# Kernel optimization log

Measured on AMD Instinct MI355X. Metric: run time of the kernel, lower is better.

The kernel has to match this reference:

```python
import jax, jax.numpy as jnp
import numpy as np

N_NODES = 100000

def _gcn_norm(edge_index, num_nodes):
    # PyG GCNConv: add self-loops, symmetric normalization deg^-1/2 A_hat deg^-1/2
    loop = jnp.arange(num_nodes, dtype=edge_index.dtype)
    src = jnp.concatenate([edge_index[0], loop])  # [E+N]
    dst = jnp.concatenate([edge_index[1], loop])  # [E+N]
    deg = jax.ops.segment_sum(jnp.ones(dst.shape[0], jnp.float32), dst, num_segments=num_nodes)
    dis = jnp.where(deg > 0, jax.lax.rsqrt(deg), 0.0)
    norm = dis[src] * dis[dst]  # [E+N]
    return src, dst, norm

def _gcn_layer(x, W, b, src, dst, norm, num_nodes):
    xw = x @ W                                   # [N, H] dense GEMM first (out_dim <= in_dim)
    msg = xw[src] * norm[:, None]                # gather + scale per edge
    out = jax.ops.segment_sum(msg, dst, num_segments=num_nodes)  # scatter-add
    return out + b

def setup_inputs() -> dict:
    key = jax.random.key(0)
    ks = jax.random.split(key, 6)
    E = 1600000
    return {
        "x": jax.random.normal(ks[0], (N_NODES, 512), jnp.float32),
        "edge_index": jax.random.randint(ks[1], (2, E), 0, N_NODES, dtype=jnp.int64),
        "W1": jax.random.normal(ks[2], (512, 256), jnp.float32) * 0.04,
        "b1": jnp.zeros((256,), jnp.float32),
        "W2": jax.random.normal(ks[3], (256, 256), jnp.float32) * 0.06,
        "b2": jnp.zeros((256,), jnp.float32),
        "fc_w": jax.random.normal(ks[4], (256, 128), jnp.float32) * 0.06,
        "fc_b": jnp.zeros((128,), jnp.float32),
    }

def reference(x, edge_index, W1, b1, W2, b2, fc_w, fc_b):
    src, dst, norm = _gcn_norm(edge_index, N_NODES)
    h = jax.nn.relu(_gcn_layer(x, W1, b1, src, dst, norm, N_NODES))
    h = jax.nn.relu(_gcn_layer(h, W2, b2, src, dst, norm, N_NODES))
    return h @ fc_w + fc_b
```

## Files before the change

kernel.cpp:

```cpp
#include <hip/hip_runtime.h>


#define N_NODES 100000
constexpr int D_IN  = 512;
constexpr int D_H   = 256;
constexpr int D_OUT = 128;

typedef _Float16 f16x8 __attribute__((ext_vector_type(8)));
typedef _Float16 f16x4 __attribute__((ext_vector_type(4)));
typedef float f32x4 __attribute__((ext_vector_type(4)));


__global__ __launch_bounds__(256) void deg_count_k(const int* __restrict__ dst,
                                                   int* __restrict__ deg, int E) {
  int i = blockIdx.x * 256 + threadIdx.x;
  if (i < E) atomicAdd(&deg[dst[i]], 1);
}

__global__ __launch_bounds__(256) void dis_k(const int* __restrict__ deg,
                                             float* __restrict__ dis, int n) {
  int i = blockIdx.x * 256 + threadIdx.x;
  if (i < n) dis[i] = rsqrtf((float)deg[i] + 1.0f);
}

__global__ __launch_bounds__(256) void scan1_k(const int* __restrict__ deg,
                                               int* __restrict__ off,
                                               int* __restrict__ bsum, int n) {
  __shared__ int ts[256];
  const int tid = threadIdx.x;
  const int base = blockIdx.x * 1024 + tid * 4;
  int v[4];
#pragma unroll
  for (int t = 0; t < 4; ++t) v[t] = (base + t < n) ? deg[base + t] : 0;
  const int tot = v[0] + v[1] + v[2] + v[3];
  ts[tid] = tot;
  __syncthreads();
  for (int o = 1; o < 256; o <<= 1) {
    int t = (tid >= o) ? ts[tid - o] : 0;
    __syncthreads();
    ts[tid] += t;
    __syncthreads();
  }
  int run = ts[tid] - tot;
#pragma unroll
  for (int t = 0; t < 4; ++t) {
    if (base + t < n) off[base + t] = run;
    run += v[t];
  }
  if (tid == 255) bsum[blockIdx.x] = ts[255];
}

__global__ __launch_bounds__(128) void scan2_k(int* __restrict__ bsum, int nb) {
  __shared__ int ts[128];
  const int tid = threadIdx.x;
  const int v = (tid < nb) ? bsum[tid] : 0;
  ts[tid] = v;
  __syncthreads();
  for (int o = 1; o < 128; o <<= 1) {
    int t = (tid >= o) ? ts[tid - o] : 0;
    __syncthreads();
    ts[tid] += t;
    __syncthreads();
  }
  if (tid < nb) bsum[tid] = ts[tid] - v;
}

__global__ __launch_bounds__(256) void scan3_k(int* __restrict__ off,
                                               const int* __restrict__ bsum,
                                               int n, int E) {
  int i = blockIdx.x * 256 + threadIdx.x;
  if (i < n) off[i] += bsum[i >> 10];
  if (i == 0) off[n] = E;
}

__global__ __launch_bounds__(256) void fill_k(const int* __restrict__ src,
                                              const int* __restrict__ dst,
                                              const int* __restrict__ off,
                                              int* __restrict__ cursor,
                                              int* __restrict__ ssorted, int E) {
  int e = blockIdx.x * 256 + threadIdx.x;
  if (e < E) {
    int d = dst[e];
    int p = off[d] + atomicAdd(&cursor[d], 1);
    ssorted[p] = src[e];
  }
}

__global__ __launch_bounds__(256) void wtrans_k(const float* __restrict__ W,
                                                _Float16* __restrict__ T,
                                                int K, int logN) {
  int i = blockIdx.x * 256 + threadIdx.x;
  if (i >= (K << logN)) return;
  int k = i >> logN, n = i & ((1 << logN) - 1);
  T[(size_t)n * K + k] = (_Float16)W[i];
}

template<int BN, bool CONVERT_A, bool OUT_Y>
__global__ __launch_bounds__(512, 4) void gemm_pipe_k(
    const float* __restrict__ Af32,
    const _Float16* __restrict__ A16,
    const _Float16* __restrict__ Bt,
    const float* __restrict__ bias,
    const float* __restrict__ dis,
    float* __restrict__ C,
    _Float16* __restrict__ Y,
    int M, int K) {
  constexpr int BM = 128, BK = 32;
  constexpr int FN = BN / 64;
  constexpr int NB = BN / 128;
  constexpr int EPAD = 4;

  __shared__ __align__(16) _Float16 smem[2 * (BM + BN) * BK];
  _Float16* As = smem;
  _Float16* Bs = smem + 2 * BM * BK;
  float* epi = (float*)smem;

  const int tid  = threadIdx.x;
  const int wid  = tid >> 6, lane = tid & 63;
  const int wm   = wid >> 2, wn = wid & 3;
  const int l15  = lane & 15, l16 = lane >> 4;
  const int row0 = blockIdx.y * BM;

  f32x4 acc[4][FN];
#pragma unroll
  for (int i = 0; i < 4; ++i)
#pragma unroll
    for (int j = 0; j < FN; ++j) acc[i][j] = (f32x4){0.f, 0.f, 0.f, 0.f};

  const int arow = tid >> 2;
  const int ak8  = (tid & 3) << 3;
  float4 areg0, areg1;
  f16x8  a16reg;
  f16x8  breg[NB];

  const int nsteps = K >> 5;

  auto stage_load = [&](int kt) {
    const int gr = row0 + arow;
    if constexpr (CONVERT_A) {
      if (gr < M) {
        const float* ap = Af32 + (size_t)gr * K + kt + ak8;
        areg0 = *(const float4*)ap;
        areg1 = *(const float4*)(ap + 4);
      } else {
        areg0 = make_float4(0.f, 0.f, 0.f, 0.f);
        areg1 = make_float4(0.f, 0.f, 0.f, 0.f);
      }
    } else {
      if (gr < M) a16reg = *(const f16x8*)(A16 + (size_t)gr * K + kt + ak8);
      else        a16reg = (f16x8){0, 0, 0, 0, 0, 0, 0, 0};
    }
#pragma unroll
    for (int it = 0; it < NB; ++it) {
      int idx = tid + it * 512;
      int n = idx >> 2, k8 = (idx & 3) << 3;
      breg[it] = *(const f16x8*)(Bt + (size_t)n * K + kt + k8);
    }
  };

  auto stage_write = [&](int buf) {
    _Float16* as = As + buf * (BM * BK);
    _Float16* bs = Bs + buf * (BN * BK);
    if constexpr (CONVERT_A) {
      f16x8 v;
      v[0] = (_Float16)areg0.x; v[1] = (_Float16)areg0.y;
      v[2] = (_Float16)areg0.z; v[3] = (_Float16)areg0.w;
      v[4] = (_Float16)areg1.x; v[5] = (_Float16)areg1.y;
      v[6] = (_Float16)areg1.z; v[7] = (_Float16)areg1.w;
      *(f16x8*)&as[arow * BK + ak8] = v;
    } else {
      *(f16x8*)&as[arow * BK + ak8] = a16reg;
    }
#pragma unroll
    for (int it = 0; it < NB; ++it) {
      int idx = tid + it * 512;
      int n = idx >> 2, k8 = (idx & 3) << 3;
      *(f16x8*)&bs[n * BK + k8] = breg[it];
    }
  };

  stage_load(0);
  stage_write(0);
  if (nsteps > 1) stage_load(BK);
  __syncthreads();

  for (int t = 0; t < nsteps; ++t) {
    const int buf = t & 1;
    const _Float16* as = As + buf * (BM * BK);
    const _Float16* bs = Bs + buf * (BN * BK);

    f16x8 a[4], b[FN];
#pragma unroll
    for (int i = 0; i < 4; ++i)
      a[i] = *(const f16x8*)&as[(wm * 64 + i * 16 + l15) * BK + l16 * 8];
#pragma unroll
    for (int j = 0; j < FN; ++j)
      b[j] = *(const f16x8*)&bs[(wn * (FN * 16) + j * 16 + l15) * BK + l16 * 8];

#pragma unroll
    for (int i = 0; i < 4; ++i)
#pragma unroll
      for (int j = 0; j < FN; ++j)
        acc[i][j] = __builtin_amdgcn_mfma_f32_16x16x32_f16(a[i], b[j], acc[i][j], 0, 0, 0);

    if (t + 1 < nsteps) {
      stage_write(buf ^ 1);
      if (t + 2 < nsteps) stage_load((t + 2) << 5);
    }
    __syncthreads();
  }

  constexpr int ESTR = BN + EPAD;
  constexpr int CPT  = BN / 16;
#pragma unroll
  for (int c = 0; c < 4; ++c) {
    if (wm == (c >> 1)) {
      const int ib = (c & 1) * 2;
#pragma unroll
      for (int ii = 0; ii < 2; ++ii) {
        const int i = ib + ii;
#pragma unroll
        for (int j = 0; j < FN; ++j) {
          const int col = wn * (FN * 16) + j * 16 + l15;
#pragma unroll
          for (int r = 0; r < 4; ++r) {
            const int lrow = ii * 16 + l16 * 4 + r;
            epi[lrow * ESTR + col] = acc[i][j][r];
          }
        }
      }
    }
    __syncthreads();
    {
      const int lrow = tid >> 4;
      const int grow = row0 + c * 32 + lrow;
      const int colb = (tid & 15) * CPT;
      if (grow < M) {
        float v[CPT];
#pragma unroll
        for (int q = 0; q < CPT; q += 4)
          *(float4*)&v[q] = *(const float4*)&epi[lrow * ESTR + colb + q];
        if constexpr (OUT_Y) {
          const float dv = dis[grow];
          f16x8 o[CPT / 8];
#pragma unroll
          for (int q = 0; q < CPT; ++q) o[q >> 3][q & 7] = (_Float16)(v[q] * dv);
#pragma unroll
          for (int q = 0; q < CPT / 8; ++q)
            *(f16x8*)(Y + (size_t)grow * BN + colb + q * 8) = o[q];
        } else {
#pragma unroll
          for (int q = 0; q < CPT; ++q) v[q] += bias[colb + q];
#pragma unroll
          for (int q = 0; q < CPT; q += 4)
            *(float4*)(C + (size_t)grow * BN + colb + q) = *(const float4*)&v[q];
        }
      }
    }
    __syncthreads();
  }
}

__global__ __launch_bounds__(256) void gather_k(const _Float16* __restrict__ y,
                                                const int* __restrict__ ssorted,
                                                const int* __restrict__ off,
                                                const float* __restrict__ dis,
                                                const float* __restrict__ bias,
                                                _Float16* __restrict__ h,
                                                int n) {
  const int gid = blockIdx.x * 256 + threadIdx.x;
  const int v = gid >> 6, lane = gid & 63;
  if (v >= n) return;

  const float dv = dis[v];
  const int fo = lane * 4;

  f16x4 sv = *(const f16x4*)(y + (size_t)v * 256 + fo);
  float4 acc = make_float4((float)sv[0], (float)sv[1], (float)sv[2], (float)sv[3]);

  const int beg = off[v], end = off[v + 1];
  const int ne = end - beg;

  for (int j0 = 0; j0 < ne; j0 += 64) {
    const int rem = ne - j0;
    const int cnt = rem < 64 ? rem : 64;
    int s_l = 0;
    if (lane < cnt) s_l = ssorted[beg + j0 + lane];

    int k = 0;
    for (; k + 8 <= cnt; k += 8) {
      f16x4 yv[8];
#pragma unroll
      for (int u = 0; u < 8; ++u) {
        const int s = __shfl(s_l, k + u);
        yv[u] = *(const f16x4*)(y + (size_t)s * 256 + fo);
      }
#pragma unroll
      for (int u = 0; u < 8; ++u) {
        acc.x += (float)yv[u][0];
        acc.y += (float)yv[u][1];
        acc.z += (float)yv[u][2];
        acc.w += (float)yv[u][3];
      }
    }
    for (; k < cnt; ++k) {
      const int s = __shfl(s_l, k);
      const f16x4 yv = *(const f16x4*)(y + (size_t)s * 256 + fo);
      acc.x += (float)yv[0];
      acc.y += (float)yv[1];
      acc.z += (float)yv[2];
      acc.w += (float)yv[3];
    }
  }

  const float4 b = *(const float4*)(bias + fo);
  f16x4 o;
  o[0] = (_Float16)fmaxf(fmaf(dv, acc.x, b.x), 0.f);
  o[1] = (_Float16)fmaxf(fmaf(dv, acc.y, b.y), 0.f);
  o[2] = (_Float16)fmaxf(fmaf(dv, acc.z, b.z), 0.f);
  o[3] = (_Float16)fmaxf(fmaf(dv, acc.w, b.w), 0.f);
  *(f16x4*)(h + (size_t)v * 256 + fo) = o;
}

extern "C" void kernel_launch(void* const* d_in, const int* in_sizes, int n_in,
                              void* d_out, int out_size, void* d_ws, size_t ws_size,
                              hipStream_t stream) {
  const float* x    = (const float*)d_in[0];
  const int*   ei   = (const int*)d_in[1];
  const float* W1   = (const float*)d_in[2];
  const float* b1   = (const float*)d_in[3];
  const float* W2   = (const float*)d_in[4];
  const float* b2   = (const float*)d_in[5];
  const float* fc_w = (const float*)d_in[6];
  const float* fc_b = (const float*)d_in[7];
  float* out = (float*)d_out;

  const int E = in_sizes[1] / 2;
  const int* src = ei;
  const int* dst = ei + E;
  const int N = N_NODES;

  char* p = (char*)d_ws;
  int*   deg     = (int*)p;            p += (size_t)N * 4;
  int*   cursor  = (int*)p;            p += (size_t)N * 4;
  float* dis     = (float*)p;          p += (size_t)N * 4;
  int*   off     = (int*)p;            p += (size_t)(N + 1) * 4;
  int*   ssorted = (int*)p;            p += (size_t)E * 4;
  int*   bsum    = (int*)p;            p += 512;
  p = (char*)(((size_t)p + 255) & ~(size_t)255);
  _Float16* w1t = (_Float16*)p;        p += (size_t)D_H   * D_IN * 2;
  _Float16* w2t = (_Float16*)p;        p += (size_t)D_H   * D_H  * 2;
  _Float16* fct = (_Float16*)p;        p += (size_t)D_OUT * D_H  * 2;
  p = (char*)(((size_t)p + 255) & ~(size_t)255);
  _Float16* y16 = (_Float16*)p;        p += (size_t)N * D_H * 2;
  _Float16* h16 = (_Float16*)p;        p += (size_t)N * D_H * 2;

  wtrans_k<<<(D_IN * D_H + 255) / 256, 256, 0, stream>>>(W1, w1t, D_IN, 8);
  wtrans_k<<<(D_H * D_H + 255) / 256, 256, 0, stream>>>(W2, w2t, D_H, 8);
  wtrans_k<<<(D_H * D_OUT + 255) / 256, 256, 0, stream>>>(fc_w, fct, D_H, 7);

  const int NB1 = (N + 1023) / 1024;
  hipMemsetAsync(deg, 0, 2 * N * sizeof(int), stream);
  deg_count_k<<<(E + 255) / 256, 256, 0, stream>>>(dst, deg, E);
  dis_k<<<(N + 255) / 256, 256, 0, stream>>>(deg, dis, N);
  scan1_k<<<NB1, 256, 0, stream>>>(deg, off, bsum, N);
  scan2_k<<<1, 128, 0, stream>>>(bsum, NB1);
  scan3_k<<<(N + 255) / 256, 256, 0, stream>>>(off, bsum, N, E);
  fill_k<<<(E + 255) / 256, 256, 0, stream>>>(src, dst, off, cursor, ssorted, E);

  const int node_wave_blocks = (N * 64 + 255) / 256;
  const int MB = (N + 127) / 128;
  const dim3 gg(1, MB);

  gemm_pipe_k<256, true, true><<<gg, 512, 0, stream>>>(
      x, nullptr, w1t, nullptr, dis, nullptr, y16, N, D_IN);
  gather_k<<<node_wave_blocks, 256, 0, stream>>>(y16, ssorted, off, dis, b1, h16, N);

  gemm_pipe_k<256, false, true><<<gg, 512, 0, stream>>>(
      nullptr, h16, w2t, nullptr, dis, nullptr, y16, N, D_H);
  gather_k<<<node_wave_blocks, 256, 0, stream>>>(y16, ssorted, off, dis, b2, h16, N);

  gemm_pipe_k<128, false, false><<<gg, 512, 0, stream>>>(
      nullptr, h16, fct, fc_b, nullptr, out, nullptr, N, D_H);
}
```

Baseline: 534.7 us.

## Fuse preprocessing kernels, record atomic positions, and restructure GEMM double-buffer loop

Result: faster. 519.7 us (-2.8%).

```diff
diff --git a/kernel.cpp b/kernel.cpp
--- a/kernel.cpp
+++ b/kernel.cpp
@@ -12,26 +12,35 @@
 
 
 __global__ __launch_bounds__(256) void deg_count_k(const int* __restrict__ dst,
-                                                   int* __restrict__ deg, int E) {
-  int i = blockIdx.x * 256 + threadIdx.x;
-  if (i < E) atomicAdd(&deg[dst[i]], 1);
-}
-
-__global__ __launch_bounds__(256) void dis_k(const int* __restrict__ deg,
-                                             float* __restrict__ dis, int n) {
-  int i = blockIdx.x * 256 + threadIdx.x;
-  if (i < n) dis[i] = rsqrtf((float)deg[i] + 1.0f);
+                                                   int* __restrict__ deg,
+                                                   int* __restrict__ pe, int E) {
+  int i = (blockIdx.x * 256 + threadIdx.x) * 4;
+  if (i + 3 < E) {
+    int4 d = *(const int4*)(dst + i);
+    int4 p;
+    p.x = atomicAdd(&deg[d.x], 1);
+    p.y = atomicAdd(&deg[d.y], 1);
+    p.z = atomicAdd(&deg[d.z], 1);
+    p.w = atomicAdd(&deg[d.w], 1);
+    *(int4*)(pe + i) = p;
+  } else {
+    for (int t = i; t < E; ++t) pe[t] = atomicAdd(&deg[dst[t]], 1);
+  }
 }
 
 __global__ __launch_bounds__(256) void scan1_k(const int* __restrict__ deg,
                                                int* __restrict__ off,
-                                               int* __restrict__ bsum, int n) {
+                                               int* __restrict__ bsum,
+                                               float* __restrict__ dis, int n) {
   __shared__ int ts[256];
   const int tid = threadIdx.x;
   const int base = blockIdx.x * 1024 + tid * 4;
   int v[4];
 #pragma unroll
   for (int t = 0; t < 4; ++t) v[t] = (base + t < n) ? deg[base + t] : 0;
+#pragma unroll
+  for (int t = 0; t < 4; ++t)
+    if (base + t < n) dis[base + t] = rsqrtf((float)v[t] + 1.0f);
   const int tot = v[0] + v[1] + v[2] + v[3];
   ts[tid] = tot;
   __syncthreads();
@@ -65,34 +74,48 @@
   if (tid < nb) bsum[tid] = ts[tid] - v;
 }
 
-__global__ __launch_bounds__(256) void scan3_k(int* __restrict__ off,
-                                               const int* __restrict__ bsum,
-                                               int n, int E) {
-  int i = blockIdx.x * 256 + threadIdx.x;
-  if (i < n) off[i] += bsum[i >> 10];
-  if (i == 0) off[n] = E;
-}
-
 __global__ __launch_bounds__(256) void fill_k(const int* __restrict__ src,
                                               const int* __restrict__ dst,
+                                              const int* __restrict__ pe,
                                               const int* __restrict__ off,
-                                              int* __restrict__ cursor,
+                                              const int* __restrict__ bsum,
                                               int* __restrict__ ssorted, int E) {
-  int e = blockIdx.x * 256 + threadIdx.x;
-  if (e < E) {
-    int d = dst[e];
-    int p = off[d] + atomicAdd(&cursor[d], 1);
-    ssorted[p] = src[e];
-  }
-}
-
-__global__ __launch_bounds__(256) void wtrans_k(const float* __restrict__ W,
-                                                _Float16* __restrict__ T,
-                                                int K, int logN) {
+  int i = (blockIdx.x * 256 + threadIdx.x) * 4;
+  if (i + 3 < E) {
+    int4 s = *(const int4*)(src + i);
+    int4 d = *(const int4*)(dst + i);
+    int4 p = *(const int4*)(pe + i);
+    ssorted[off[d.x] + bsum[d.x >> 10] + p.x] = s.x;
+    ssorted[off[d.y] + bsum[d.y >> 10] + p.y] = s.y;
+    ssorted[off[d.z] + bsum[d.z >> 10] + p.z] = s.z;
+    ssorted[off[d.w] + bsum[d.w >> 10] + p.w] = s.w;
+  } else {
+    for (int t = i; t < E; ++t) {
+      int d = dst[t];
+      ssorted[off[d] + bsum[d >> 10] + pe[t]] = src[t];
+    }
+  }
+}
+
+__global__ __launch_bounds__(256) void wtrans_all_k(const float* __restrict__ W1,
+                                                    const float* __restrict__ W2,
+                                                    const float* __restrict__ FC,
+                                                    _Float16* __restrict__ w1t,
+                                                    _Float16* __restrict__ w2t,
+                                                    _Float16* __restrict__ fct) {
   int i = blockIdx.x * 256 + threadIdx.x;
-  if (i >= (K << logN)) return;
-  int k = i >> logN, n = i & ((1 << logN) - 1);
-  T[(size_t)n * K + k] = (_Float16)W[i];
+  if (i < 131072) {
+    int k = i >> 8, n = i & 255;
+    w1t[(size_t)n * 512 + k] = (_Float16)W1[i];
+  } else if (i < 196608) {
+    int j = i - 131072;
+    int k = j >> 8, n = j & 255;
+    w2t[(size_t)n * 256 + k] = (_Float16)W2[j];
+  } else if (i < 229376) {
+    int j = i - 196608;
+    int k = j >> 7, n = j & 127;
+    fct[(size_t)n * 256 + k] = (_Float16)FC[j];
+  }
 }
 
 template<int BN, bool CONVERT_A, bool OUT_Y>
@@ -108,7 +131,7 @@
   constexpr int BM = 128, BK = 32;
   constexpr int FN = BN / 64;
   constexpr int NB = BN / 128;
-  constexpr int EPAD = 4;
+  constexpr int EPAD = 8;
 
   __shared__ __align__(16) _Float16 smem[2 * (BM + BN) * BK];
   _Float16* As = smem;
@@ -129,86 +152,92 @@
 
   const int arow = tid >> 2;
   const int ak8  = (tid & 3) << 3;
-  float4 areg0, areg1;
-  f16x8  a16reg;
-  f16x8  breg[NB];
+  const int gr   = row0 + arow;
+  const int brow0 = tid >> 2;
+  const int bk8   = (tid & 3) << 3;
+
+  float4 aA0, aB0, aA1, aB1;
+  f16x8  hA0, hA1;
+  f16x8  b0A, b0B, b1A, b1B;
 
   const int nsteps = K >> 5;
 
-  auto stage_load = [&](int kt) {
-    const int gr = row0 + arow;
-    if constexpr (CONVERT_A) {
-      if (gr < M) {
-        const float* ap = Af32 + (size_t)gr * K + kt + ak8;
-        areg0 = *(const float4*)ap;
-        areg1 = *(const float4*)(ap + 4);
-      } else {
-        areg0 = make_float4(0.f, 0.f, 0.f, 0.f);
-        areg1 = make_float4(0.f, 0.f, 0.f, 0.f);
-      }
-    } else {
-      if (gr < M) a16reg = *(const f16x8*)(A16 + (size_t)gr * K + kt + ak8);
-      else        a16reg = (f16x8){0, 0, 0, 0, 0, 0, 0, 0};
-    }
-#pragma unroll
-    for (int it = 0; it < NB; ++it) {
-      int idx = tid + it * 512;
-      int n = idx >> 2, k8 = (idx & 3) << 3;
-      breg[it] = *(const f16x8*)(Bt + (size_t)n * K + kt + k8);
-    }
-  };
-
-  auto stage_write = [&](int buf) {
-    _Float16* as = As + buf * (BM * BK);
-    _Float16* bs = Bs + buf * (BN * BK);
-    if constexpr (CONVERT_A) {
-      f16x8 v;
-      v[0] = (_Float16)areg0.x; v[1] = (_Float16)areg0.y;
-      v[2] = (_Float16)areg0.z; v[3] = (_Float16)areg0.w;
-      v[4] = (_Float16)areg1.x; v[5] = (_Float16)areg1.y;
-      v[6] = (_Float16)areg1.z; v[7] = (_Float16)areg1.w;
-      *(f16x8*)&as[arow * BK + ak8] = v;
-    } else {
-      *(f16x8*)&as[arow * BK + ak8] = a16reg;
-    }
-#pragma unroll
-    for (int it = 0; it < NB; ++it) {
-      int idx = tid + it * 512;
-      int n = idx >> 2, k8 = (idx & 3) << 3;
-      *(f16x8*)&bs[n * BK + k8] = breg[it];
-    }
-  };
-
-  stage_load(0);
-  stage_write(0);
-  if (nsteps > 1) stage_load(BK);
+#define LD_SET(kt, aA, aB, hA, bA, bB)                                         \
+  {                                                                            \
+    if constexpr (CONVERT_A) {                                                 \
+      if (gr < M) {                                                            \
+        const float* ap = Af32 + (size_t)gr * K + (kt) + ak8;                  \
+        aA = *(const float4*)ap;                                               \
+        aB = *(const float4*)(ap + 4);                                         \
+      } else {                                                                 \
+        aA = make_float4(0.f, 0.f, 0.f, 0.f);                                  \
+        aB = make_float4(0.f, 0.f, 0.f, 0.f);                                  \
+      }                                                                        \
+    } else {                                                                   \
+      if (gr < M) hA = *(const f16x8*)(A16 + (size_t)gr * K + (kt) + ak8);     \
+      else        hA = (f16x8){0, 0, 0, 0, 0, 0, 0, 0};                        \
+    }                                                                          \
+    bA = *(const f16x8*)(Bt + (size_t)brow0 * K + (kt) + bk8);                 \
+    if constexpr (NB > 1)                                                      \
+      bB = *(const f16x8*)(Bt + (size_t)(brow0 + 128) * K + (kt) + bk8);       \
+  }
+
+#define WR_SET(buf, aA, aB, hA, bA, bB)                                        \
+  {                                                                            \
+    _Float16* as = As + (buf) * (BM * BK);                                     \
+    _Float16* bs = Bs + (buf) * (BN * BK);                                     \
+    if constexpr (CONVERT_A) {                                                 \
+      f16x8 v;                                                                 \
+      v[0] = (_Float16)aA.x; v[1] = (_Float16)aA.y;                            \
+      v[2] = (_Float16)aA.z; v[3] = (_Float16)aA.w;                            \
+      v[4] = (_Float16)aB.x; v[5] = (_Float16)aB.y;                            \
+      v[6] = (_Float16)aB.z; v[7] = (_Float16)aB.w;                            \
+      *(f16x8*)&as[arow * BK + ak8] = v;                                       \
+    } else {                                                                   \
+      *(f16x8*)&as[arow * BK + ak8] = hA;                                      \
+    }                                                                          \
+    *(f16x8*)&bs[brow0 * BK + bk8] = bA;                                       \
+    if constexpr (NB > 1) *(f16x8*)&bs[(brow0 + 128) * BK + bk8] = bB;         \
+  }
+
+#define COMPUTE(buf)                                                           \
+  {                                                                            \
+    const _Float16* as = As + (buf) * (BM * BK);                               \
+    const _Float16* bs = Bs + (buf) * (BN * BK);                               \
+    f16x8 a[4], b[FN];                                                         \
+    _Pragma("unroll")                                                          \
+    for (int i = 0; i < 4; ++i)                                                \
+      a[i] = *(const f16x8*)&as[(wm * 64 + i * 16 + l15) * BK + l16 * 8];      \
+    _Pragma("unroll")                                                          \
+    for (int j = 0; j < FN; ++j)                                               \
+      b[j] = *(const f16x8*)&bs[(wn * (FN * 16) + j * 16 + l15) * BK + l16 * 8]; \
+    _Pragma("unroll")                                                          \
+    for (int i = 0; i < 4; ++i)                                                \
+      _Pragma("unroll")                                                        \
+      for (int j = 0; j < FN; ++j)                                             \
+        acc[i][j] = __builtin_amdgcn_mfma_f32_16x16x32_f16(a[i], b[j], acc[i][j], 0, 0, 0); \
+  }
+
+  LD_SET(0, aA0, aB0, hA0, b0A, b0B);
+  WR_SET(0, aA0, aB0, hA0, b0A, b0B);
+  LD_SET(BK, aA1, aB1, hA1, b1A, b1B);
   __syncthreads();
 
-  for (int t = 0; t < nsteps; ++t) {
-    const int buf = t & 1;
-    const _Float16* as = As + buf * (BM * BK);
-    const _Float16* bs = Bs + buf * (BN * BK);
-
-    f16x8 a[4], b[FN];
-#pragma unroll
-    for (int i = 0; i < 4; ++i)
-      a[i] = *(const f16x8*)&as[(wm * 64 + i * 16 + l15) * BK + l16 * 8];
-#pragma unroll
-    for (int j = 0; j < FN; ++j)
-      b[j] = *(const f16x8*)&bs[(wn * (FN * 16) + j * 16 + l15) * BK + l16 * 8];
-
-#pragma unroll
-    for (int i = 0; i < 4; ++i)
-#pragma unroll
-      for (int j = 0; j < FN; ++j)
-        acc[i][j] = __builtin_amdgcn_mfma_f32_16x16x32_f16(a[i], b[j], acc[i][j], 0, 0, 0);
-
-    if (t + 1 < nsteps) {
-      stage_write(buf ^ 1);
-      if (t + 2 < nsteps) stage_load((t + 2) << 5);
-    }
-    __syncthreads();
-  }
+  for (int tt = 0; tt < nsteps; tt += 2) {
+    if (tt + 2 < nsteps) LD_SET((tt + 2) * BK, aA0, aB0, hA0, b0A, b0B);
+    COMPUTE(0);
+    if (tt + 1 < nsteps) WR_SET(1, aA1, aB1, hA1, b1A, b1B);
+    __syncthreads();
+    if (tt + 1 < nsteps) {
+      if (tt + 3 < nsteps) LD_SET((tt + 3) * BK, aA1, aB1, hA1, b1A, b1B);
+      COMPUTE(1);
+      if (tt + 2 < nsteps) WR_SET(0, aA0, aB0, hA0, b0A, b0B);
+      __syncthreads();
+    }
+  }
+#undef LD_SET
+#undef WR_SET
+#undef COMPUTE
 
   constexpr int ESTR = BN + EPAD;
   constexpr int CPT  = BN / 16;
@@ -264,10 +293,11 @@
 __global__ __launch_bounds__(256) void gather_k(const _Float16* __restrict__ y,
                                                 const int* __restrict__ ssorted,
                                                 const int* __restrict__ off,
+                                                const int* __restrict__ bsum,
                                                 const float* __restrict__ dis,
                                                 const float* __restrict__ bias,
                                                 _Float16* __restrict__ h,
-                                                int n) {
+                                                int n, int E) {
   const int gid = blockIdx.x * 256 + threadIdx.x;
   const int v = gid >> 6, lane = gid & 63;
   if (v >= n) return;
@@ -278,7 +308,8 @@
   f16x4 sv = *(const f16x4*)(y + (size_t)v * 256 + fo);
   float4 acc = make_float4((float)sv[0], (float)sv[1], (float)sv[2], (float)sv[3]);
 
-  const int beg = off[v], end = off[v + 1];
+  const int beg = off[v] + bsum[v >> 10];
+  const int end = (v + 1 < n) ? (off[v + 1] + bsum[(v + 1) >> 10]) : E;
   const int ne = end - beg;
 
   for (int j0 = 0; j0 < ne; j0 += 64) {
@@ -342,9 +373,9 @@
 
   char* p = (char*)d_ws;
   int*   deg     = (int*)p;            p += (size_t)N * 4;
-  int*   cursor  = (int*)p;            p += (size_t)N * 4;
   float* dis     = (float*)p;          p += (size_t)N * 4;
   int*   off     = (int*)p;            p += (size_t)(N + 1) * 4;
+  int*   pe      = (int*)p;            p += (size_t)E * 4;
   int*   ssorted = (int*)p;            p += (size_t)E * 4;
   int*   bsum    = (int*)p;            p += 512;
   p = (char*)(((size_t)p + 255) & ~(size_t)255);
@@ -355,18 +386,15 @@
   _Float16* y16 = (_Float16*)p;        p += (size_t)N * D_H * 2;
   _Float16* h16 = (_Float16*)p;        p += (size_t)N * D_H * 2;
 
-  wtrans_k<<<(D_IN * D_H + 255) / 256, 256, 0, stream>>>(W1, w1t, D_IN, 8);
-  wtrans_k<<<(D_H * D_H + 255) / 256, 256, 0, stream>>>(W2, w2t, D_H, 8);
-  wtrans_k<<<(D_H * D_OUT + 255) / 256, 256, 0, stream>>>(fc_w, fct, D_H, 7);
+  wtrans_all_k<<<896, 256, 0, stream>>>(W1, W2, fc_w, w1t, w2t, fct);
 
   const int NB1 = (N + 1023) / 1024;
-  hipMemsetAsync(deg, 0, 2 * N * sizeof(int), stream);
-  deg_count_k<<<(E + 255) / 256, 256, 0, stream>>>(dst, deg, E);
-  dis_k<<<(N + 255) / 256, 256, 0, stream>>>(deg, dis, N);
-  scan1_k<<<NB1, 256, 0, stream>>>(deg, off, bsum, N);
+  const int EB4 = ((E + 3) / 4 + 255) / 256;
+  hipMemsetAsync(deg, 0, N * sizeof(int), stream);
+  deg_count_k<<<EB4, 256, 0, stream>>>(dst, deg, pe, E);
+  scan1_k<<<NB1, 256, 0, stream>>>(deg, off, bsum, dis, N);
   scan2_k<<<1, 128, 0, stream>>>(bsum, NB1);
-  scan3_k<<<(N + 255) / 256, 256, 0, stream>>>(off, bsum, N, E);
-  fill_k<<<(E + 255) / 256, 256, 0, stream>>>(src, dst, off, cursor, ssorted, E);
+  fill_k<<<EB4, 256, 0, stream>>>(src, dst, pe, off, bsum, ssorted, E);
 
   const int node_wave_blocks = (N * 64 + 255) / 256;
   const int MB = (N + 127) / 128;
@@ -374,11 +402,11 @@
 
   gemm_pipe_k<256, true, true><<<gg, 512, 0, stream>>>(
       x, nullptr, w1t, nullptr, dis, nullptr, y16, N, D_IN);
-  gather_k<<<node_wave_blocks, 256, 0, stream>>>(y16, ssorted, off, dis, b1, h16, N);
+  gather_k<<<node_wave_blocks, 256, 0, stream>>>(y16, ssorted, off, bsum, dis, b1, h16, N, E);
 
   gemm_pipe_k<256, false, true><<<gg, 512, 0, stream>>>(
       nullptr, h16, w2t, nullptr, dis, nullptr, y16, N, D_H);
-  gather_k<<<node_wave_blocks, 256, 0, stream>>>(y16, ssorted, off, dis, b2, h16, N);
+  gather_k<<<node_wave_blocks, 256, 0, stream>>>(y16, ssorted, off, bsum, dis, b2, h16, N, E);
 
   gemm_pipe_k<128, false, false><<<gg, 512, 0, stream>>>(
       nullptr, h16, fct, fc_b, nullptr, out, nullptr, N, D_H);
```
